# Kernel optimization log

Measured on AMD Instinct MI355X. Metric: run time of the kernel, lower is better.

The kernel has to match this reference:

```python
import jax, jax.numpy as jnp
import numpy as np

HIDDEN = 1024
HEADS = 16
HEAD = HIDDEN // HEADS  # 64, rotary_emb_dim == head dim
B = 8
S = 1024  # max_seqlen; all sequences full length
WINDOW = (64, 64)  # sliding_window=128 -> (64, 64)
ROPE_BASE = 10000.0


def _rope_cos_sin(seqlen, dim, base):
    inv_freq = 1.0 / (base ** (jnp.arange(0, dim, 2, dtype=jnp.float32) / dim))
    t = jnp.arange(seqlen, dtype=jnp.float32)
    freqs = jnp.outer(t, inv_freq)  # [S, dim/2]
    return jnp.cos(freqs), jnp.sin(freqs)


def _apply_rope(x, cos, sin):
    # x: [B, S, H, D], non-interleaved rotary over full head dim
    d2 = cos.shape[-1]
    x1, x2 = x[..., :d2], x[..., d2:]
    c = cos[None, :, None, :]
    s = sin[None, :, None, :]
    return jnp.concatenate([x1 * c - x2 * s, x2 * c + x1 * s], axis=-1)


def setup_inputs() -> dict:
    key = jax.random.key(0)
    k1, k2, k3 = jax.random.split(key, 3)
    hidden_states = jax.random.normal(k1, (B * S, HIDDEN), dtype=jnp.float32)
    cu_seqlens = jnp.arange(B + 1, dtype=jnp.int32) * S
    indices = jnp.arange(B * S, dtype=jnp.int32)
    attn_mask = jnp.ones((B, S), dtype=jnp.int32)
    Wqkv = jax.random.normal(k2, (3 * HIDDEN, HIDDEN), dtype=jnp.float32) * 0.02
    Wo = jax.random.normal(k3, (HIDDEN, HIDDEN), dtype=jnp.float32) * 0.02
    return {
        'hidden_states': hidden_states,
        'cu_seqlens': cu_seqlens,
        'max_seqlen': S,
        'indices': indices,
        'attn_mask': attn_mask,
        'Wqkv': Wqkv,
        'Wo': Wo,
    }


def reference(hidden_states, cu_seqlens, max_seqlen, indices, attn_mask, Wqkv, Wo):
    # QKV projection on unpadded tokens: [T, 3*H*D]
    qkv = hidden_states @ Wqkv.T
    qkv = qkv.reshape(B, S, 3, HEADS, HEAD)
    # Rotary positions reset per sequence; all sequences are full length S.
    cos, sin = _rope_cos_sin(S, HEAD, ROPE_BASE)
    q = _apply_rope(qkv[:, :, 0], cos, sin)
    k = _apply_rope(qkv[:, :, 1], cos, sin)
    v = qkv[:, :, 2]
    scores = jnp.einsum('bshd,bthd->bhst', q, k) / jnp.sqrt(jnp.float32(HEAD))
    # sliding-window mask: key j visible to query i iff i-left <= j <= i+right
    i = jnp.arange(S)[:, None]
    j = jnp.arange(S)[None, :]
    win = (j >= i - WINDOW[0]) & (j <= i + WINDOW[1])  # [S, S]
    key_mask = attn_mask.astype(bool)[:, None, None, :]  # [B,1,1,S]
    mask = win[None, None, :, :] & key_mask
    scores = jnp.where(mask, scores, jnp.finfo(scores.dtype).min)
    probs = jax.nn.softmax(scores, axis=-1)
    attn = jnp.einsum('bhst,bthd->bshd', probs, v).reshape(B * S, HIDDEN)
    return attn @ Wo.T
```

## Files before the change

kernel.cpp:

```cpp
#include <hip/hip_runtime.h>


typedef __attribute__((ext_vector_type(8))) short short8;
typedef __attribute__((ext_vector_type(4))) float f32x4;

#define SEQ   1024
#define NHEAD 16
#define HEADD 64
#define NTOK  8192

__device__ __forceinline__ unsigned short f2bf(float x) {
  unsigned u = __float_as_uint(x);
  u += 0x7fffu + ((u >> 16) & 1u);
  return (unsigned short)(u >> 16);
}

__device__ __forceinline__ void gload_lds16(const void* g, void* l) {
  __builtin_amdgcn_global_load_lds((__attribute__((address_space(1))) void*)(g),
                                   (__attribute__((address_space(3))) void*)(l),
                                   16, 0, 0);
}

__global__ __launch_bounds__(256) void prep(
    const float* __restrict__ hidden, const float* __restrict__ Wqkv,
    const float* __restrict__ Wo,
    unsigned short* __restrict__ hb, unsigned short* __restrict__ wqb,
    unsigned short* __restrict__ wob, float2* __restrict__ tab) {
  int bid = blockIdx.x;
  const float* in; unsigned short* out; int i;
  if (bid < 8192)       { in = hidden; out = hb;  i = bid * 256 + threadIdx.x; }
  else if (bid < 11264) { in = Wqkv;   out = wqb; i = (bid - 8192) * 256 + threadIdx.x; }
  else if (bid < 12288) { in = Wo;     out = wob; i = (bid - 11264) * 256 + threadIdx.x; }
  else {
    int j = (bid - 12288) * 256 + threadIdx.x;
    int s = j >> 5, d = j & 31;
    float inv = exp2f(-(float)d * 0.41524101186092034f);
    float sn, cs;
    sincosf((float)s * inv, &sn, &cs);
    tab[j] = make_float2(cs, sn);
    return;
  }
  float4 v = ((const float4*)in)[i];
  ushort4 o;
  o.x = f2bf(v.x); o.y = f2bf(v.y); o.z = f2bf(v.z); o.w = f2bf(v.w);
  ((ushort4*)out)[i] = o;
}

__global__ __launch_bounds__(256) void gemm_qkv_rope(
    const unsigned short* __restrict__ A,
    const unsigned short* __restrict__ W,
    const float2* __restrict__ tab,
    unsigned short* __restrict__ qb,
    unsigned short* __restrict__ kb,
    unsigned short* __restrict__ vt)
{
  __shared__ unsigned short As[2][128 * 64];
  __shared__ unsigned short Bs[2][128 * 64];
  const int tid  = threadIdx.x;
  const int wave = tid >> 6, lane = tid & 63;
  const int quad = lane >> 4, l15 = lane & 15;
  const int bid  = blockIdx.x;
  const int xcd  = bid & 7, idx = bid >> 3;
  const int rb   = xcd * 8 + (idx & 7);
  const int cb   = idx >> 3;
  const int row0 = rb * 128;
  const int col0 = cb * 128;
  const int mrow = (wave >> 1) * 64;
  const int ncol = (wave & 1) * 64;
  const int l7x8 = (l15 & 7) * 8;

  f32x4 acc[4][4];
#pragma unroll
  for (int i = 0; i < 4; i++)
#pragma unroll
    for (int j = 0; j < 4; j++) acc[i][j] = (f32x4){0.f, 0.f, 0.f, 0.f};

  auto stage = [&](int bi, int k0) {
#pragma unroll
    for (int i = 0; i < 4; i++) {
      int p = i * 256 + tid;
      int r = p >> 3, c = p & 7;
      int cs = c ^ (r & 7);
      gload_lds16(A + (size_t)(row0 + r) * 1024 + k0 + cs * 8, &As[bi][p * 8]);
      gload_lds16(W + (size_t)(col0 + r) * 1024 + k0 + cs * 8, &Bs[bi][p * 8]);
    }
  };

  stage(0, 0);
  __syncthreads();
  int buf = 0;
  for (int k0 = 0; k0 < 1024; k0 += 64) {
    if (k0 + 64 < 1024) stage(buf ^ 1, k0 + 64);
#pragma unroll
    for (int kk = 0; kk < 2; kk++) {
      const int qs8 = ((kk * 4 + quad) * 8) ^ l7x8;
      short8 af[4], bfr[4];
#pragma unroll
      for (int mt = 0; mt < 4; mt++)
        af[mt] = *(const short8*)&As[buf][(mrow + mt * 16 + l15) * 64 + qs8];
#pragma unroll
      for (int nt = 0; nt < 4; nt++)
        bfr[nt] = *(const short8*)&Bs[buf][(ncol + nt * 16 + l15) * 64 + qs8];
#pragma unroll
      for (int mt = 0; mt < 4; mt++)
#pragma unroll
        for (int nt = 0; nt < 4; nt++)
          acc[mt][nt] = __builtin_amdgcn_mfma_f32_16x16x32_bf16(af[mt], bfr[nt],
                                                                acc[mt][nt], 0, 0, 0);
    }
    __syncthreads();
    buf ^= 1;
  }

  const int colw  = col0 + ncol;
  const int which = colw >> 10;
  const int h     = (colw >> 6) & 15;
  const int rowg  = row0 + mrow;

  if (which == 2) {
#pragma unroll
    for (int mt = 0; mt < 4; mt++) {
      int rbase = rowg + mt * 16 + quad * 4;
      int b = rbase >> 10, s = rbase & 1023;
#pragma unroll
      for (int c = 0; c < 4; c++) {
        int d = c * 16 + l15;
        ushort4 o;
        o.x = f2bf(acc[mt][c][0]); o.y = f2bf(acc[mt][c][1]);
        o.z = f2bf(acc[mt][c][2]); o.w = f2bf(acc[mt][c][3]);
        *(ushort4*)&vt[((size_t)((b * 16 + h) * 64 + d)) * 1024 + s] = o;
      }
    }
  } else {
    unsigned short* dst = (which == 0) ? qb : kb;
    const float scale = (which == 0) ? 0.125f : 1.0f;
#pragma unroll
    for (int mt = 0; mt < 4; mt++) {
#pragma unroll
      for (int r = 0; r < 4; r++) {
        int row = rowg + mt * 16 + quad * 4 + r;
        int b = row >> 10, s = row & 1023;
        size_t base = (size_t)((b * 16 + h) * 1024 + s) * 64;
        float2 t0 = tab[s * 32 + l15];
        float2 t1 = tab[s * 32 + 16 + l15];
        float x1a = acc[mt][0][r], x2a = acc[mt][2][r];
        float x1b = acc[mt][1][r], x2b = acc[mt][3][r];
        dst[base + l15]           = f2bf((x1a * t0.x - x2a * t0.y) * scale);
        dst[base + 32 + l15]      = f2bf((x2a * t0.x + x1a * t0.y) * scale);
        dst[base + 16 + l15]      = f2bf((x1b * t1.x - x2b * t1.y) * scale);
        dst[base + 48 + l15]      = f2bf((x2b * t1.x + x1b * t1.y) * scale);
      }
    }
  }
}

__global__ __launch_bounds__(256) void attn_win(
    const unsigned short* __restrict__ qb,
    const unsigned short* __restrict__ kb,
    const unsigned short* __restrict__ vt,
    const int* __restrict__ am,
    unsigned short* __restrict__ ob)
{
  __shared__ unsigned short Ks[192 * 68];
  __shared__ unsigned short Vs[64 * 196];
  __shared__ unsigned short smask[192];

  const int tid  = threadIdx.x;
  const int wave = tid >> 6, lane = tid & 63;
  const int quad = lane >> 4, l15 = lane & 15;
  const int b  = blockIdx.x >> 4, h = blockIdx.x & 15;
  const int qs = blockIdx.y * 64;
  const size_t hb = (size_t)(b * 16 + h);
  const unsigned short* Qg = qb + hb * SEQ * 64;
  const unsigned short* Kg = kb + hb * SEQ * 64;
  const unsigned short* Vg = vt + hb * 64 * SEQ;
  const int t0 = qs - 64;

#pragma unroll
  for (int i = 0; i < 6; i++) {
    int p = i * 256 + tid;
    int r = p >> 3, c = p & 7;
    int t = t0 + r; t = t < 0 ? 0 : (t > 1023 ? 1023 : t);
    *(short8*)&Ks[r * 68 + c * 8] = *(const short8*)&Kg[(size_t)t * 64 + c * 8];
  }
#pragma unroll
  for (int i = 0; i < 6; i++) {
    int p = i * 256 + tid;
    int d = p / 24, c = p % 24;
    int t = t0 + c * 8; t = t < 0 ? 0 : (t > 1016 ? 1016 : t);
    *(short8*)&Vs[d * 196 + c * 8] = *(const short8*)&Vg[(size_t)d * SEQ + t];
  }
  if (tid < 192) {
    int t = t0 + tid;
    smask[tid] = (t >= 0 && t < SEQ) ? (unsigned short)(am[b * SEQ + t] != 0) : 0;
  }
  __syncthreads();

  const int qw = qs + wave * 16;
  short8 qf0 = *(const short8*)&Qg[(size_t)(qw + l15) * 64 + quad * 8];
  short8 qf1 = *(const short8*)&Qg[(size_t)(qw + l15) * 64 + 32 + quad * 8];

  f32x4 sc[12];
#pragma unroll
  for (int tt = 0; tt < 12; tt++) {
    short8 b0 = *(const short8*)&Ks[(tt * 16 + l15) * 68 + quad * 8];
    short8 b1 = *(const short8*)&Ks[(tt * 16 + l15) * 68 + 32 + quad * 8];
    f32x4 a = (f32x4){0.f, 0.f, 0.f, 0.f};
    a = __builtin_amdgcn_mfma_f32_16x16x32_bf16(qf0, b0, a, 0, 0, 0);
    a = __builtin_amdgcn_mfma_f32_16x16x32_bf16(qf1, b1, a, 0, 0, 0);
    sc[tt] = a;
  }

  float lrow[4];
#pragma unroll
  for (int r = 0; r < 4; r++) {
    int i = qw + quad * 4 + r;
    float sum = 0.f;
#pragma unroll
    for (int tt = 0; tt < 12; tt++) {
      int t = t0 + tt * 16 + l15;
      bool ok = (t >= i - 64) && (t <= i + 64) && smask[tt * 16 + l15];
      float p = ok ? __expf(sc[tt][r]) : 0.f;
      sc[tt][r] = p;
      sum += p;
    }
#pragma unroll
    for (int off = 1; off < 16; off <<= 1) sum += __shfl_xor(sum, off);
    lrow[r] = sum;
  }

  __syncthreads();
  unsigned short* Pw = &Ks[wave * (16 * 196)];
#pragma unroll
  for (int tt = 0; tt < 12; tt++)
#pragma unroll
    for (int r = 0; r < 4; r++)
      Pw[(quad * 4 + r) * 196 + tt * 16 + l15] = f2bf(sc[tt][r]);
  __syncthreads();

  f32x4 o[4];
#pragma unroll
  for (int dt = 0; dt < 4; dt++) o[dt] = (f32x4){0.f, 0.f, 0.f, 0.f};
#pragma unroll
  for (int kt = 0; kt < 6; kt++) {
    short8 pf = *(const short8*)&Pw[l15 * 196 + kt * 32 + quad * 8];
#pragma unroll
    for (int dt = 0; dt < 4; dt++) {
      short8 vf = *(const short8*)&Vs[(dt * 16 + l15) * 196 + kt * 32 + quad * 8];
      o[dt] = __builtin_amdgcn_mfma_f32_16x16x32_bf16(pf, vf, o[dt], 0, 0, 0);
    }
  }

#pragma unroll
  for (int r = 0; r < 4; r++) {
    float inv = 1.f / lrow[r];
    int tok = b * SEQ + qw + quad * 4 + r;
    size_t base = (size_t)tok * 1024 + h * 64;
#pragma unroll
    for (int dt = 0; dt < 4; dt++)
      ob[base + dt * 16 + l15] = f2bf(o[dt][r] * inv);
  }
}

__global__ __launch_bounds__(256) void gemm_out(
    const unsigned short* __restrict__ A,
    const unsigned short* __restrict__ W,
    float* __restrict__ out)
{
  __shared__ unsigned short As[2][128 * 64];
  __shared__ unsigned short Bs[2][64 * 64];
  const int tid  = threadIdx.x;
  const int wave = tid >> 6, lane = tid & 63;
  const int quad = lane >> 4, l15 = lane & 15;
  const int bid  = blockIdx.x;
  const int xcd  = bid & 7, idx = bid >> 3;
  const int row0 = (xcd * 8 + (idx & 7)) * 128;
  const int col0 = (idx >> 3) * 64;
  const int mrow = (wave >> 1) * 64;
  const int ncol = (wave & 1) * 32;
  const int l7x8 = (l15 & 7) * 8;

  f32x4 acc[4][2];
#pragma unroll
  for (int i = 0; i < 4; i++)
#pragma unroll
    for (int j = 0; j < 2; j++) acc[i][j] = (f32x4){0.f, 0.f, 0.f, 0.f};

  auto stage = [&](int bi, int k0) {
#pragma unroll
    for (int i = 0; i < 4; i++) {
      int p = i * 256 + tid;
      int r = p >> 3, c = p & 7;
      int cs = c ^ (r & 7);
      gload_lds16(A + (size_t)(row0 + r) * 1024 + k0 + cs * 8, &As[bi][p * 8]);
    }
#pragma unroll
    for (int i = 0; i < 2; i++) {
      int p = i * 256 + tid;
      int r = p >> 3, c = p & 7;
      int cs = c ^ (r & 7);
      gload_lds16(W + (size_t)(col0 + r) * 1024 + k0 + cs * 8, &Bs[bi][p * 8]);
    }
  };

  stage(0, 0);
  __syncthreads();
  int buf = 0;
  for (int k0 = 0; k0 < 1024; k0 += 64) {
    if (k0 + 64 < 1024) stage(buf ^ 1, k0 + 64);
#pragma unroll
    for (int kk = 0; kk < 2; kk++) {
      const int qs8 = ((kk * 4 + quad) * 8) ^ l7x8;
      short8 af[4], bfr[2];
#pragma unroll
      for (int mt = 0; mt < 4; mt++)
        af[mt] = *(const short8*)&As[buf][(mrow + mt * 16 + l15) * 64 + qs8];
#pragma unroll
      for (int nt = 0; nt < 2; nt++)
        bfr[nt] = *(const short8*)&Bs[buf][(ncol + nt * 16 + l15) * 64 + qs8];
#pragma unroll
      for (int mt = 0; mt < 4; mt++)
#pragma unroll
        for (int nt = 0; nt < 2; nt++)
          acc[mt][nt] = __builtin_amdgcn_mfma_f32_16x16x32_bf16(af[mt], bfr[nt],
                                                                acc[mt][nt], 0, 0, 0);
    }
    __syncthreads();
    buf ^= 1;
  }

  const int colw = col0 + ncol;
  const int rowg = row0 + mrow;
#pragma unroll
  for (int mt = 0; mt < 4; mt++)
#pragma unroll
    for (int r = 0; r < 4; r++) {
      int row = rowg + mt * 16 + quad * 4 + r;
#pragma unroll
      for (int nt = 0; nt < 2; nt++)
        out[(size_t)row * 1024 + colw + nt * 16 + l15] = acc[mt][nt][r];
    }
}

extern "C" void kernel_launch(void* const* d_in, const int* in_sizes, int n_in,
                              void* d_out, int out_size, void* d_ws, size_t ws_size,
                              hipStream_t stream) {
  const float* hidden = (const float*)d_in[0];
  const int*   am     = (const int*)d_in[4];
  const float* Wqkv   = (const float*)d_in[5];
  const float* Wo     = (const float*)d_in[6];
  float* out = (float*)d_out;

  char* ws = (char*)d_ws;
  unsigned short* hb  = (unsigned short*)(ws);
  unsigned short* wqb = (unsigned short*)(ws + (size_t)(16 << 20));
  unsigned short* wob = (unsigned short*)(ws + (size_t)(22 << 20));
  unsigned short* qbf = (unsigned short*)(ws + (size_t)(24 << 20));
  unsigned short* kbf = (unsigned short*)(ws + (size_t)(40 << 20));
  unsigned short* vtb = (unsigned short*)(ws + (size_t)(56 << 20));
  float2*         tab = (float2*)(ws + (size_t)(72 << 20));
  unsigned short* ab  = hb;

  prep<<<12416, 256, 0, stream>>>(hidden, Wqkv, Wo, hb, wqb, wob, tab);

  gemm_qkv_rope<<<1536, 256, 0, stream>>>(hb, wqb, tab, qbf, kbf, vtb);

  dim3 g2(128, 16);
  attn_win<<<g2, 256, 0, stream>>>(qbf, kbf, vtb, am, ab);

  gemm_out<<<1024, 256, 0, stream>>>(ab, wob, out);
}
```

Measured before the change: 221.8 us.

## Restructure GEMM main loops with explicit vmcnt waits and split barriers

Rewrites the QKV and output projection GEMM K-loops so that the next tile's global-to-LDS loads are issued, then only the previous tile's loads are waited on with a partial s_waitcnt vmcnt. All LDS fragments for both k-halves are read into registers before a second barrier, and the MFMAs then run without holding the buffer. The aim is to overlap the prefetch with compute and avoid the full vmcnt(0) drain that __syncthreads implies. In exchange it uses more registers for fragments and depends on the hand-counted vmcnt values matching the number of issued loads.

```diff
diff --git a/kernel.cpp b/kernel.cpp
--- a/kernel.cpp
+++ b/kernel.cpp
@@ -87,28 +87,43 @@
   };
 
   stage(0, 0);
-  __syncthreads();
   int buf = 0;
-  for (int k0 = 0; k0 < 1024; k0 += 64) {
-    if (k0 + 64 < 1024) stage(buf ^ 1, k0 + 64);
-#pragma unroll
-    for (int kk = 0; kk < 2; kk++) {
-      const int qs8 = ((kk * 4 + quad) * 8) ^ l7x8;
-      short8 af[4], bfr[4];
-#pragma unroll
-      for (int mt = 0; mt < 4; mt++)
-        af[mt] = *(const short8*)&As[buf][(mrow + mt * 16 + l15) * 64 + qs8];
+  for (int t = 0; t < 16; ++t) {
+    if (t + 1 < 16) {
+      stage(buf ^ 1, (t + 1) * 64);
+      asm volatile("s_waitcnt vmcnt(8)" ::: "memory");
+    } else {
+      asm volatile("s_waitcnt vmcnt(0)" ::: "memory");
+    }
+    __builtin_amdgcn_s_barrier();
+
+    short8 af0[4], bf0[4], af1[4], bf1[4];
+#pragma unroll
+    for (int mt = 0; mt < 4; mt++) {
+      af0[mt] = *(const short8*)&As[buf][(mrow + mt * 16 + l15) * 64 + ((quad * 8) ^ l7x8)];
+      af1[mt] = *(const short8*)&As[buf][(mrow + mt * 16 + l15) * 64 + (((4 + quad) * 8) ^ l7x8)];
+    }
+#pragma unroll
+    for (int nt = 0; nt < 4; nt++) {
+      bf0[nt] = *(const short8*)&Bs[buf][(ncol + nt * 16 + l15) * 64 + ((quad * 8) ^ l7x8)];
+      bf1[nt] = *(const short8*)&Bs[buf][(ncol + nt * 16 + l15) * 64 + (((4 + quad) * 8) ^ l7x8)];
+    }
+    asm volatile("s_waitcnt lgkmcnt(0)" ::: "memory");
+    __builtin_amdgcn_sched_barrier(0);
+    __builtin_amdgcn_s_barrier();
+
+#pragma unroll
+    for (int mt = 0; mt < 4; mt++)
 #pragma unroll
       for (int nt = 0; nt < 4; nt++)
-        bfr[nt] = *(const short8*)&Bs[buf][(ncol + nt * 16 + l15) * 64 + qs8];
-#pragma unroll
-      for (int mt = 0; mt < 4; mt++)
-#pragma unroll
-        for (int nt = 0; nt < 4; nt++)
-          acc[mt][nt] = __builtin_amdgcn_mfma_f32_16x16x32_bf16(af[mt], bfr[nt],
-                                                                acc[mt][nt], 0, 0, 0);
-    }
-    __syncthreads();
+        acc[mt][nt] = __builtin_amdgcn_mfma_f32_16x16x32_bf16(af0[mt], bf0[nt],
+                                                              acc[mt][nt], 0, 0, 0);
+#pragma unroll
+    for (int mt = 0; mt < 4; mt++)
+#pragma unroll
+      for (int nt = 0; nt < 4; nt++)
+        acc[mt][nt] = __builtin_amdgcn_mfma_f32_16x16x32_bf16(af1[mt], bf1[nt],
+                                                              acc[mt][nt], 0, 0, 0);
     buf ^= 1;
   }
 
@@ -304,28 +319,43 @@
   };
 
   stage(0, 0);
-  __syncthreads();
   int buf = 0;
-  for (int k0 = 0; k0 < 1024; k0 += 64) {
-    if (k0 + 64 < 1024) stage(buf ^ 1, k0 + 64);
-#pragma unroll
-    for (int kk = 0; kk < 2; kk++) {
-      const int qs8 = ((kk * 4 + quad) * 8) ^ l7x8;
-      short8 af[4], bfr[2];
-#pragma unroll
-      for (int mt = 0; mt < 4; mt++)
-        af[mt] = *(const short8*)&As[buf][(mrow + mt * 16 + l15) * 64 + qs8];
+  for (int t = 0; t < 16; ++t) {
+    if (t + 1 < 16) {
+      stage(buf ^ 1, (t + 1) * 64);
+      asm volatile("s_waitcnt vmcnt(6)" ::: "memory");
+    } else {
+      asm volatile("s_waitcnt vmcnt(0)" ::: "memory");
+    }
+    __builtin_amdgcn_s_barrier();
+
+    short8 af0[4], bf0[2], af1[4], bf1[2];
+#pragma unroll
+    for (int mt = 0; mt < 4; mt++) {
+      af0[mt] = *(const short8*)&As[buf][(mrow + mt * 16 + l15) * 64 + ((quad * 8) ^ l7x8)];
+      af1[mt] = *(const short8*)&As[buf][(mrow + mt * 16 + l15) * 64 + (((4 + quad) * 8) ^ l7x8)];
+    }
+#pragma unroll
+    for (int nt = 0; nt < 2; nt++) {
+      bf0[nt] = *(const short8*)&Bs[buf][(ncol + nt * 16 + l15) * 64 + ((quad * 8) ^ l7x8)];
+      bf1[nt] = *(const short8*)&Bs[buf][(ncol + nt * 16 + l15) * 64 + (((4 + quad) * 8) ^ l7x8)];
+    }
+    asm volatile("s_waitcnt lgkmcnt(0)" ::: "memory");
+    __builtin_amdgcn_sched_barrier(0);
+    __builtin_amdgcn_s_barrier();
+
+#pragma unroll
+    for (int mt = 0; mt < 4; mt++)
 #pragma unroll
       for (int nt = 0; nt < 2; nt++)
-        bfr[nt] = *(const short8*)&Bs[buf][(ncol + nt * 16 + l15) * 64 + qs8];
-#pragma unroll
-      for (int mt = 0; mt < 4; mt++)
-#pragma unroll
-        for (int nt = 0; nt < 2; nt++)
-          acc[mt][nt] = __builtin_amdgcn_mfma_f32_16x16x32_bf16(af[mt], bfr[nt],
-                                                                acc[mt][nt], 0, 0, 0);
-    }
-    __syncthreads();
+        acc[mt][nt] = __builtin_amdgcn_mfma_f32_16x16x32_bf16(af0[mt], bf0[nt],
+                                                              acc[mt][nt], 0, 0, 0);
+#pragma unroll
+    for (int mt = 0; mt < 4; mt++)
+#pragma unroll
+      for (int nt = 0; nt < 2; nt++)
+        acc[mt][nt] = __builtin_amdgcn_mfma_f32_16x16x32_bf16(af1[mt], bf1[nt],
+                                                              acc[mt][nt], 0, 0, 0);
     buf ^= 1;
   }
 
```

Result: slower. 231.7 us (+4.5%).
